# Optimization experiments

Measured on AMD Instinct MI355X. Metric: run time of the kernel, lower is better.

## Reference

```python
import jax, jax.numpy as jnp
import numpy as np

# Central first difference with zero (same) padding along `axis`:
# out[i] = f[i+1] - f[i-1], zeros outside the domain (conv3d w/ [-1,0,1] kernel, same pad).
def d1(f, axis):
    pad = [(0, 0)] * f.ndim
    pad[axis] = (1, 1)
    fp = jnp.pad(f, pad)
    hi = tuple(slice(2, None) if a == axis else slice(None) for a in range(f.ndim))
    lo = tuple(slice(None, -2) if a == axis else slice(None) for a in range(f.ndim))
    return fp[hi] - fp[lo]

# Second difference: f[i+1] - 2 f[i] + f[i-1], zero padded.
def d2(f, axis):
    pad = [(0, 0)] * f.ndim
    pad[axis] = (1, 1)
    fp = jnp.pad(f, pad)
    hi = tuple(slice(2, None) if a == axis else slice(None) for a in range(f.ndim))
    lo = tuple(slice(None, -2) if a == axis else slice(None) for a in range(f.ndim))
    return fp[hi] - 2.0 * f + fp[lo]

AX_T, AX_X, AX_Y = 2, 3, 4  # [B, C, T, X, Y]
D_t = lambda f: d1(f, AX_T)
D_x = lambda f: d1(f, AX_X)
D_y = lambda f: d1(f, AX_Y)
D_xx_yy = lambda f: d2(f, AX_X) + d2(f, AX_Y)  # Laplacian in x,y


def setup_inputs() -> dict:
    key = jax.random.key(0)
    B, C, T, X, Y = 8, 4, 64, 128, 128
    vars_ = jax.random.normal(key, (B, C, T, X, Y), dtype=jnp.float32)
    return {
        "vars": vars_,
        "dx": jnp.float32(0.0078),
        "dt": jnp.float32(0.05),
        "eta": jnp.float32(0.01),
        "zeta": jnp.float32(0.01),
    }


def reference(vars, dx, dt, eta, zeta):
    rho = vars[:, 0:1]
    u = vars[:, 1:2]
    v = vars[:, 2:3]
    p = vars[:, 3:4]

    # mass residual (final, rescaled assignment in the torch source;
    # `self.rho` there is the continuity-eq density field rho)
    mass = (D_t(rho) * dx
            + rho * (D_x(u) + D_y(v)) * dt
            + u * D_x(rho) * dt
            + v * D_y(rho) * dt)

    div = D_x(u) + D_y(v)
    bulk = zeta + eta / 3.0

    mom_x = (rho * D_t(u) * 2.0 * dx ** 2
             + u * D_x(u) * 2.0 * dt * dx
             + v * D_y(u) * 2.0 * dt * dx
             + D_x(p) * 2.0 * dt * dx
             - eta * D_xx_yy(u) * 4.0 * dt
             - bulk * D_x(div) * 2.0 * dt)
    mom_y = (rho * D_t(v) * 2.0 * dx ** 2
             + u * D_x(v) * 2.0 * dt * dx
             + v * D_y(v) * 2.0 * dt * dx
             + D_y(p) * 2.0 * dt * dx
             - eta * D_xx_yy(v) * 4.0 * dt
             - bulk * D_y(div) * 2.0 * dt)
    mom = mom_x + mom_y

    # boundary=False path: strip 1-cell boundary in t, x, y; stack residuals on channel
    inner = (Ellipsis, slice(1, -1), slice(1, -1), slice(1, -1))
    return jnp.concatenate([mass[inner], mom[inner]], axis=1)
```

## Files before the change

kernel.cpp:

```cpp
#include <hip/hip_runtime.h>


typedef float vf4 __attribute__((ext_vector_type(4)));
typedef float vf4u __attribute__((ext_vector_type(4), aligned(4)));

__device__ __forceinline__ vf4 ld4(const float* __restrict__ p) {
    return *reinterpret_cast<const vf4u*>(p);
}

#define SH(lo, hi, s) __builtin_shufflevector(lo, hi, 2 + (s), 3 + (s), 4 + (s), 5 + (s))

__global__ __launch_bounds__(256) void cns_residuals_kernel(
    const float* __restrict__ vars,
    const float* __restrict__ s_dx, const float* __restrict__ s_dt,
    const float* __restrict__ s_eta, const float* __restrict__ s_zeta,
    float* __restrict__ out)
{
    const float dx = s_dx[0], dt = s_dt[0], eta = s_eta[0], zeta = s_zeta[0];
    const float bulk = zeta + eta * (1.0f / 3.0f);
    const float c1 = 2.0f * dx * dx;
    const float c2 = 2.0f * dt * dx;
    const float c3 = 4.0f * dt;
    const float c4 = 2.0f * dt;

    const int i = blockIdx.x;
    const int xcd = i & 7;
    const int slot = i >> 3;
    const int lb = (xcd < 4) ? xcd * 977 + slot
                             : 3908 + (xcd - 4) * 976 + slot;

    const int tid = lb * 256 + threadIdx.x;
    const int j = tid & 31;
    int r = tid >> 5;
    const int xp = r % 126; r /= 126;
    const int tp = r % 62;  const int b = r / 62;
    const int x = xp + 1, t = tp + 1;
    const int yb = 1 + 4 * j;

    const size_t plane = 16384;
    const size_t cstr  = (size_t)64 * plane;

    const float* base = vars + (size_t)b * 4 * cstr + (size_t)t * plane
                      + ((size_t)x << 7) + yb;
    const float* R0 = base;
    const float* U0 = base + cstr;
    const float* V0 = base + 2 * cstr;
    const float* P0 = base + 3 * cstr;

    const float mLo = (j == 0)  ? 0.0f : 1.0f;
    const float mHi = (j == 31) ? 0.0f : 1.0f;

#define WIN(ptr, off, lo, hi) \
    vf4 lo = ld4((ptr) + (off) - 2); vf4 hi = ld4((ptr) + (off) + 2); \
    lo[0] *= mLo; hi[1] *= mHi; hi[2] *= mHi; hi[3] *= mHi;

    WIN(R0, 0,    r0lo, r0hi)
    WIN(U0, 0,    u0lo, u0hi)
    WIN(U0, 128,  uplo, uphi)
    WIN(U0, -128, umlo, umhi)
    WIN(V0, 0,    v0lo, v0hi)
    WIN(V0, 128,  vplo, vphi)
    WIN(V0, -128, vmlo, vmhi)
    WIN(P0, 0,    p0lo, p0hi)
#undef WIN

    const vf4 rxp = ld4(R0 + 128), rxm = ld4(R0 - 128);
    const vf4 rtp = ld4(R0 + plane), rtm = ld4(R0 - plane);
    const vf4 utp = ld4(U0 + plane), utm = ld4(U0 - plane);
    const vf4 vtp = ld4(V0 + plane), vtm = ld4(V0 - plane);
    const vf4 pxp = ld4(P0 + 128), pxm = ld4(P0 - 128);
    const vf4 zero = {0.0f, 0.0f, 0.0f, 0.0f};
    const vf4 uxp2 = (x <= 125) ? ld4(U0 + 256) : zero;
    const vf4 uxm2 = (x >= 2)   ? ld4(U0 - 256) : zero;

    const vf4 rho = SH(r0lo, r0hi, 0);
    const vf4 u   = SH(u0lo, u0hi, 0);
    const vf4 v   = SH(v0lo, v0hi, 0);

    const vf4 uxp = SH(uplo, uphi, 0), uxm = SH(umlo, umhi, 0);
    const vf4 uyp = SH(u0lo, u0hi, 1), uym = SH(u0lo, u0hi, -1);
    const vf4 vxp = SH(vplo, vphi, 0), vxm = SH(vmlo, vmhi, 0);
    const vf4 vyp = SH(v0lo, v0hi, 1), vym = SH(v0lo, v0hi, -1);

    const vf4 Dt_rho = rtp - rtm;
    const vf4 Dx_rho = rxp - rxm;
    const vf4 Dy_rho = SH(r0lo, r0hi, 1) - SH(r0lo, r0hi, -1);
    const vf4 Dx_u = uxp - uxm, Dy_u = uyp - uym;
    const vf4 Dx_v = vxp - vxm, Dy_v = vyp - vym;

    const vf4 mass = Dt_rho * dx + rho * (Dx_u + Dy_v) * dt
                   + u * Dx_rho * dt + v * Dy_rho * dt;

    const vf4 Dt_u = utp - utm, Dt_v = vtp - vtm;
    const vf4 Dx_p = pxp - pxm;
    const vf4 Dy_p = SH(p0lo, p0hi, 1) - SH(p0lo, p0hi, -1);
    const vf4 lap_u = uxp + uxm + uyp + uym - 4.0f * u;
    const vf4 lap_v = vxp + vxm + vyp + vym - 4.0f * v;

    const vf4 Dx_div = uxp2 - 2.0f * u + uxm2
                     + SH(vplo, vphi, 1) - SH(vplo, vphi, -1)
                     - SH(vmlo, vmhi, 1) + SH(vmlo, vmhi, -1);
    const vf4 Dy_div = SH(v0lo, v0hi, 2) - 2.0f * v + SH(v0lo, v0hi, -2)
                     + SH(uplo, uphi, 1) - SH(umlo, umhi, 1)
                     - SH(uplo, uphi, -1) + SH(umlo, umhi, -1);

    const vf4 mom = rho * (Dt_u + Dt_v) * c1
                  + (u * Dx_u + v * Dy_u + u * Dx_v + v * Dy_v) * c2
                  + (Dx_p + Dy_p) * c2
                  - eta * (lap_u + lap_v) * c3
                  - bulk * (Dx_div + Dy_div) * c4;

    const size_t oplane = 126 * 126;
    const size_t ocstr  = (size_t)62 * oplane;
    float* o1 = out + (size_t)b * 2 * ocstr + (size_t)tp * oplane
              + (size_t)xp * 126 + 4 * j;
    float* o2 = o1 + ocstr;
    if (j < 31) {
        __builtin_nontemporal_store(mass, reinterpret_cast<vf4u*>(o1));
        __builtin_nontemporal_store(mom,  reinterpret_cast<vf4u*>(o2));
    } else {
        __builtin_nontemporal_store(mass[0], o1);
        __builtin_nontemporal_store(mass[1], o1 + 1);
        __builtin_nontemporal_store(mom[0],  o2);
        __builtin_nontemporal_store(mom[1],  o2 + 1);
    }
}

extern "C" void kernel_launch(void* const* d_in, const int* in_sizes, int n_in,
                              void* d_out, int out_size, void* d_ws, size_t ws_size,
                              hipStream_t stream) {
    const float* vars   = (const float*)d_in[0];
    const float* s_dx   = (const float*)d_in[1];
    const float* s_dt   = (const float*)d_in[2];
    const float* s_eta  = (const float*)d_in[3];
    const float* s_zeta = (const float*)d_in[4];
    float* out = (float*)d_out;

    const int grid = 7812;
    hipLaunchKernelGGL(cns_residuals_kernel, dim3(grid), dim3(256), 0, stream,
                       vars, s_dx, s_dt, s_eta, s_zeta, out);
}
```

Measured before the change: 39.98 us.

## Compute two x-rows per thread to reuse stencil window loads

```diff
diff --git a/kernel.cpp b/kernel.cpp
--- a/kernel.cpp
+++ b/kernel.cpp
@@ -8,7 +8,9 @@
     return *reinterpret_cast<const vf4u*>(p);
 }
 
-#define SH(lo, hi, s) __builtin_shufflevector(lo, hi, 2 + (s), 3 + (s), 4 + (s), 5 + (s))
+struct Win { vf4 lo, hi; };
+
+#define SH(w, s) __builtin_shufflevector((w).lo, (w).hi, 2 + (s), 3 + (s), 4 + (s), 5 + (s))
 
 __global__ __launch_bounds__(256) void cns_residuals_kernel(
     const float* __restrict__ vars,
@@ -26,22 +28,21 @@
     const int i = blockIdx.x;
     const int xcd = i & 7;
     const int slot = i >> 3;
-    const int lb = (xcd < 4) ? xcd * 977 + slot
-                             : 3908 + (xcd - 4) * 976 + slot;
+    const int lb = ((xcd < 2) ? xcd * 489 : 978 + (xcd - 2) * 488) + slot;
 
     const int tid = lb * 256 + threadIdx.x;
     const int j = tid & 31;
     int r = tid >> 5;
-    const int xp = r % 126; r /= 126;
+    const int xh = r % 63; r /= 63;
     const int tp = r % 62;  const int b = r / 62;
-    const int x = xp + 1, t = tp + 1;
+    const int x0 = 1 + 2 * xh, t = tp + 1;
     const int yb = 1 + 4 * j;
 
     const size_t plane = 16384;
     const size_t cstr  = (size_t)64 * plane;
 
     const float* base = vars + (size_t)b * 4 * cstr + (size_t)t * plane
-                      + ((size_t)x << 7) + yb;
+                      + ((size_t)x0 << 7) + yb;
     const float* R0 = base;
     const float* U0 = base + cstr;
     const float* V0 = base + 2 * cstr;
@@ -50,79 +51,95 @@
     const float mLo = (j == 0)  ? 0.0f : 1.0f;
     const float mHi = (j == 31) ? 0.0f : 1.0f;
 
-#define WIN(ptr, off, lo, hi) \
-    vf4 lo = ld4((ptr) + (off) - 2); vf4 hi = ld4((ptr) + (off) + 2); \
-    lo[0] *= mLo; hi[1] *= mHi; hi[2] *= mHi; hi[3] *= mHi;
+#define WIN(ptr) win_load(ptr, mLo, mHi)
+    struct L {
+        static __device__ __forceinline__ Win win_load(const float* p, float mLo, float mHi) {
+            Win w; w.lo = ld4(p - 2); w.hi = ld4(p + 2);
+            w.lo[0] *= mLo; w.hi[1] *= mHi; w.hi[2] *= mHi; w.hi[3] *= mHi;
+            return w;
+        }
+    };
+#undef WIN
+#define WIN(ptr) L::win_load((ptr), mLo, mHi)
 
-    WIN(R0, 0,    r0lo, r0hi)
-    WIN(U0, 0,    u0lo, u0hi)
-    WIN(U0, 128,  uplo, uphi)
-    WIN(U0, -128, umlo, umhi)
-    WIN(V0, 0,    v0lo, v0hi)
-    WIN(V0, 128,  vplo, vphi)
-    WIN(V0, -128, vmlo, vmhi)
-    WIN(P0, 0,    p0lo, p0hi)
-#undef WIN
+    const Win Rw0 = WIN(R0), Rw1 = WIN(R0 + 128);
+    const Win Uwm = WIN(U0 - 128), Uw0 = WIN(U0), Uw1 = WIN(U0 + 128), Uw2 = WIN(U0 + 256);
+    const Win Vwm = WIN(V0 - 128), Vw0 = WIN(V0), Vw1 = WIN(V0 + 128), Vw2 = WIN(V0 + 256);
+    const Win Pw0 = WIN(P0), Pw1 = WIN(P0 + 128);
 
-    const vf4 rxp = ld4(R0 + 128), rxm = ld4(R0 - 128);
-    const vf4 rtp = ld4(R0 + plane), rtm = ld4(R0 - plane);
-    const vf4 utp = ld4(U0 + plane), utm = ld4(U0 - plane);
-    const vf4 vtp = ld4(V0 + plane), vtm = ld4(V0 - plane);
-    const vf4 pxp = ld4(P0 + 128), pxm = ld4(P0 - 128);
     const vf4 zero = {0.0f, 0.0f, 0.0f, 0.0f};
-    const vf4 uxp2 = (x <= 125) ? ld4(U0 + 256) : zero;
-    const vf4 uxm2 = (x >= 2)   ? ld4(U0 - 256) : zero;
+    const vf4 Rc_m1 = ld4(R0 - 128), Rc_p2 = ld4(R0 + 256);
+    const vf4 Pc_m1 = ld4(P0 - 128), Pc_p2 = ld4(P0 + 256);
+    const vf4 Uc_m2 = (xh >= 1)  ? ld4(U0 - 256) : zero;
+    const vf4 Uc_p3 = (xh <= 61) ? ld4(U0 + 384) : zero;
+    const vf4 Rtp0 = ld4(R0 + plane), Rtp1 = ld4(R0 + plane + 128);
+    const vf4 Rtm0 = ld4(R0 - plane), Rtm1 = ld4(R0 - plane + 128);
+    const vf4 Utp0 = ld4(U0 + plane), Utp1 = ld4(U0 + plane + 128);
+    const vf4 Utm0 = ld4(U0 - plane), Utm1 = ld4(U0 - plane + 128);
+    const vf4 Vtp0 = ld4(V0 + plane), Vtp1 = ld4(V0 + plane + 128);
+    const vf4 Vtm0 = ld4(V0 - plane), Vtm1 = ld4(V0 - plane + 128);
 
-    const vf4 rho = SH(r0lo, r0hi, 0);
-    const vf4 u   = SH(u0lo, u0hi, 0);
-    const vf4 v   = SH(v0lo, v0hi, 0);
+    const vf4 rho0 = SH(Rw0, 0), u0c = SH(Uw0, 0), v0c = SH(Vw0, 0);
+    const vf4 uxp0 = SH(Uw1, 0), uxm0 = SH(Uwm, 0);
+    const vf4 vxp0 = SH(Vw1, 0), vxm0 = SH(Vwm, 0);
+    const vf4 uyp0 = SH(Uw0, 1), uym0 = SH(Uw0, -1);
+    const vf4 vyp0 = SH(Vw0, 1), vym0 = SH(Vw0, -1);
+    const vf4 Dxu0 = uxp0 - uxm0, Dyu0 = uyp0 - uym0;
+    const vf4 Dxv0 = vxp0 - vxm0, Dyv0 = vyp0 - vym0;
+    const vf4 mass0 = (Rtp0 - Rtm0) * dx + rho0 * (Dxu0 + Dyv0) * dt
+                    + u0c * (SH(Rw1, 0) - Rc_m1) * dt
+                    + v0c * (SH(Rw0, 1) - SH(Rw0, -1)) * dt;
+    const vf4 lapu0 = uxp0 + uxm0 + uyp0 + uym0 - 4.0f * u0c;
+    const vf4 lapv0 = vxp0 + vxm0 + vyp0 + vym0 - 4.0f * v0c;
+    const vf4 Dxdiv0 = SH(Uw2, 0) - 2.0f * u0c + Uc_m2
+                     + SH(Vw1, 1) - SH(Vw1, -1) - SH(Vwm, 1) + SH(Vwm, -1);
+    const vf4 Dydiv0 = SH(Vw0, 2) - 2.0f * v0c + SH(Vw0, -2)
+                     + SH(Uw1, 1) - SH(Uwm, 1) - SH(Uw1, -1) + SH(Uwm, -1);
+    const vf4 mom0 = rho0 * ((Utp0 - Utm0) + (Vtp0 - Vtm0)) * c1
+                   + (u0c * (Dxu0 + Dxv0) + v0c * (Dyu0 + Dyv0)) * c2
+                   + ((SH(Pw1, 0) - Pc_m1) + (SH(Pw0, 1) - SH(Pw0, -1))) * c2
+                   - eta * (lapu0 + lapv0) * c3
+                   - bulk * (Dxdiv0 + Dydiv0) * c4;
 
-    const vf4 uxp = SH(uplo, uphi, 0), uxm = SH(umlo, umhi, 0);
-    const vf4 uyp = SH(u0lo, u0hi, 1), uym = SH(u0lo, u0hi, -1);
-    const vf4 vxp = SH(vplo, vphi, 0), vxm = SH(vmlo, vmhi, 0);
-    const vf4 vyp = SH(v0lo, v0hi, 1), vym = SH(v0lo, v0hi, -1);
-
-    const vf4 Dt_rho = rtp - rtm;
-    const vf4 Dx_rho = rxp - rxm;
-    const vf4 Dy_rho = SH(r0lo, r0hi, 1) - SH(r0lo, r0hi, -1);
-    const vf4 Dx_u = uxp - uxm, Dy_u = uyp - uym;
-    const vf4 Dx_v = vxp - vxm, Dy_v = vyp - vym;
-
-    const vf4 mass = Dt_rho * dx + rho * (Dx_u + Dy_v) * dt
-                   + u * Dx_rho * dt + v * Dy_rho * dt;
-
-    const vf4 Dt_u = utp - utm, Dt_v = vtp - vtm;
-    const vf4 Dx_p = pxp - pxm;
-    const vf4 Dy_p = SH(p0lo, p0hi, 1) - SH(p0lo, p0hi, -1);
-    const vf4 lap_u = uxp + uxm + uyp + uym - 4.0f * u;
-    const vf4 lap_v = vxp + vxm + vyp + vym - 4.0f * v;
-
-    const vf4 Dx_div = uxp2 - 2.0f * u + uxm2
-                     + SH(vplo, vphi, 1) - SH(vplo, vphi, -1)
-                     - SH(vmlo, vmhi, 1) + SH(vmlo, vmhi, -1);
-    const vf4 Dy_div = SH(v0lo, v0hi, 2) - 2.0f * v + SH(v0lo, v0hi, -2)
-                     + SH(uplo, uphi, 1) - SH(umlo, umhi, 1)
-                     - SH(uplo, uphi, -1) + SH(umlo, umhi, -1);
-
-    const vf4 mom = rho * (Dt_u + Dt_v) * c1
-                  + (u * Dx_u + v * Dy_u + u * Dx_v + v * Dy_v) * c2
-                  + (Dx_p + Dy_p) * c2
-                  - eta * (lap_u + lap_v) * c3
-                  - bulk * (Dx_div + Dy_div) * c4;
+    const vf4 rho1 = SH(Rw1, 0), u1c = SH(Uw1, 0), v1c = SH(Vw1, 0);
+    const vf4 uxp1 = SH(Uw2, 0), uxm1 = SH(Uw0, 0);
+    const vf4 vxp1 = SH(Vw2, 0), vxm1 = SH(Vw0, 0);
+    const vf4 uyp1 = SH(Uw1, 1), uym1 = SH(Uw1, -1);
+    const vf4 vyp1 = SH(Vw1, 1), vym1 = SH(Vw1, -1);
+    const vf4 Dxu1 = uxp1 - uxm1, Dyu1 = uyp1 - uym1;
+    const vf4 Dxv1 = vxp1 - vxm1, Dyv1 = vyp1 - vym1;
+    const vf4 mass1 = (Rtp1 - Rtm1) * dx + rho1 * (Dxu1 + Dyv1) * dt
+                    + u1c * (Rc_p2 - SH(Rw0, 0)) * dt
+                    + v1c * (SH(Rw1, 1) - SH(Rw1, -1)) * dt;
+    const vf4 lapu1 = uxp1 + uxm1 + uyp1 + uym1 - 4.0f * u1c;
+    const vf4 lapv1 = vxp1 + vxm1 + vyp1 + vym1 - 4.0f * v1c;
+    const vf4 Dxdiv1 = Uc_p3 - 2.0f * u1c + SH(Uwm, 0)
+                     + SH(Vw2, 1) - SH(Vw2, -1) - SH(Vw0, 1) + SH(Vw0, -1);
+    const vf4 Dydiv1 = SH(Vw1, 2) - 2.0f * v1c + SH(Vw1, -2)
+                     + SH(Uw2, 1) - SH(Uw0, 1) - SH(Uw2, -1) + SH(Uw0, -1);
+    const vf4 mom1 = rho1 * ((Utp1 - Utm1) + (Vtp1 - Vtm1)) * c1
+                   + (u1c * (Dxu1 + Dxv1) + v1c * (Dyu1 + Dyv1)) * c2
+                   + ((Pc_p2 - SH(Pw0, 0)) + (SH(Pw1, 1) - SH(Pw1, -1))) * c2
+                   - eta * (lapu1 + lapv1) * c3
+                   - bulk * (Dxdiv1 + Dydiv1) * c4;
 
     const size_t oplane = 126 * 126;
     const size_t ocstr  = (size_t)62 * oplane;
     float* o1 = out + (size_t)b * 2 * ocstr + (size_t)tp * oplane
-              + (size_t)xp * 126 + 4 * j;
-    float* o2 = o1 + ocstr;
+              + (size_t)(2 * xh) * 126 + 4 * j;
+    float* o1b = o1 + 126;
+    float* o2  = o1 + ocstr;
+    float* o2b = o2 + 126;
     if (j < 31) {
-        __builtin_nontemporal_store(mass, reinterpret_cast<vf4u*>(o1));
-        __builtin_nontemporal_store(mom,  reinterpret_cast<vf4u*>(o2));
+        __builtin_nontemporal_store(mass0, reinterpret_cast<vf4u*>(o1));
+        __builtin_nontemporal_store(mass1, reinterpret_cast<vf4u*>(o1b));
+        __builtin_nontemporal_store(mom0,  reinterpret_cast<vf4u*>(o2));
+        __builtin_nontemporal_store(mom1,  reinterpret_cast<vf4u*>(o2b));
     } else {
-        __builtin_nontemporal_store(mass[0], o1);
-        __builtin_nontemporal_store(mass[1], o1 + 1);
-        __builtin_nontemporal_store(mom[0],  o2);
-        __builtin_nontemporal_store(mom[1],  o2 + 1);
+        __builtin_nontemporal_store(mass0[0], o1);      __builtin_nontemporal_store(mass0[1], o1 + 1);
+        __builtin_nontemporal_store(mass1[0], o1b);     __builtin_nontemporal_store(mass1[1], o1b + 1);
+        __builtin_nontemporal_store(mom0[0],  o2);      __builtin_nontemporal_store(mom0[1],  o2 + 1);
+        __builtin_nontemporal_store(mom1[0],  o2b);     __builtin_nontemporal_store(mom1[1],  o2b + 1);
     }
 }
 
@@ -136,7 +153,7 @@
     const float* s_zeta = (const float*)d_in[4];
     float* out = (float*)d_out;
 
-    const int grid = 7812;
+    const int grid = 3906;
     hipLaunchKernelGGL(cns_residuals_kernel, dim3(grid), dim3(256), 0, stream,
                        vars, s_dx, s_dt, s_eta, s_zeta, out);
 }
```

Result: slower. 45.12 us (+12.9%).
